# Kernel tuning notes

Hardware: AMD Instinct MI355X
Metric: run time of the kernel (lower is better)

The kernel has to match this reference:

```python
import jax, jax.numpy as jnp
import numpy as np

B, N, DIM = 2, 2048, 2048
N_HEAD, N_KV_HEAD = 32, 8
HEAD_DIM = DIM // N_HEAD  # 64
NEG_INF = -1e9


def setup_inputs() -> dict:
    key = jax.random.key(0)
    ks = jax.random.split(key, 4)
    x = jax.random.normal(ks[0], (B, N, DIM), dtype=jnp.float32)
    Wq = jax.random.normal(ks[1], (DIM, N_HEAD * HEAD_DIM), dtype=jnp.float32) * (DIM ** -0.5)
    Wkv = jax.random.normal(ks[2], (DIM, 2 * N_KV_HEAD * HEAD_DIM), dtype=jnp.float32) * (DIM ** -0.5)
    Wo = jax.random.normal(ks[3], (N_HEAD * HEAD_DIM, DIM), dtype=jnp.float32) * (DIM ** -0.5)
    # RoPE angles: freqs = 1/theta^(2i/d), angle[p, i] = p * freqs[i]
    freqs = 1.0 / (10000.0 ** (jnp.arange(0, HEAD_DIM, 2, dtype=jnp.float32) / HEAD_DIM))
    angles = jnp.arange(N, dtype=jnp.float32)[:, None] * freqs[None, :]  # (N, HEAD_DIM//2)
    rope_cos = jnp.cos(angles)
    rope_sin = jnp.sin(angles)
    # additive causal mask (n, n)
    mask = jnp.where(jnp.tril(jnp.ones((N, N), dtype=bool)), 0.0, NEG_INF).astype(jnp.float32)
    return {"x": x, "Wq": Wq, "Wkv": Wkv, "Wo": Wo, "rope_cos": rope_cos, "rope_sin": rope_sin, "mask": mask, "start_pos": 0}


def apply_rope(x, cos, sin):
    # x: (b, n, h, d); cos/sin: (n, d//2). Complex mult on interleaved pairs.
    xr = x.reshape(*x.shape[:-1], HEAD_DIM // 2, 2)
    xe, xo = xr[..., 0], xr[..., 1]
    c = cos[None, :, None, :]
    s = sin[None, :, None, :]
    yr = xe * c - xo * s
    yi = xe * s + xo * c
    return jnp.stack([yr, yi], axis=-1).reshape(x.shape)


def reference(x, Wq, Wkv, Wo, rope_cos, rope_sin, mask, start_pos):
    b, n, _ = x.shape
    q = (x @ Wq).reshape(b, n, N_HEAD, HEAD_DIM)
    kv = (x @ Wkv).reshape(b, n, 2, N_KV_HEAD, HEAD_DIM)
    k, v = kv[:, :, 0], kv[:, :, 1]
    q = apply_rope(q, rope_cos, rope_sin)
    k = apply_rope(k, rope_cos, rope_sin)
    # repeat kv heads: 'b n h d -> b n (r h) d'
    r = N_HEAD // N_KV_HEAD
    k = jnp.tile(k, (1, 1, r, 1))
    v = jnp.tile(v, (1, 1, r, 1))
    scale = HEAD_DIM ** -0.5
    attn = jnp.einsum('bnhd,bmhd->bhnm', q, k) * scale + mask[None, None]
    attn = jax.nn.softmax(attn, axis=-1)
    out = jnp.einsum('bhnm,bmhd->bnhd', attn, v).reshape(b, n, N_HEAD * HEAD_DIM)
    return out @ Wo
```

## Files before the change

kernel.cpp:

```cpp
#include <hip/hip_runtime.h>


#define BSZ  2
#define NSEQ 2048
#define DIMD 2048
#define NH   32
#define NKV  8
#define HD   64
#define TK   32

typedef __bf16 bf16x8 __attribute__((ext_vector_type(8)));
typedef __bf16 bf16x4 __attribute__((ext_vector_type(4)));
typedef __bf16 bf16x2 __attribute__((ext_vector_type(2)));
typedef float  floatx4 __attribute__((ext_vector_type(4)));

#define MFMA16(a, b, c) __builtin_amdgcn_mfma_f32_16x16x32_bf16(a, b, c, 0, 0, 0)

#define WAITV(n) asm volatile("s_waitcnt vmcnt(" #n ")" ::: "memory")

__device__ __forceinline__ void barrier_nodrain() {
    asm volatile("" ::: "memory");
    __builtin_amdgcn_sched_barrier(0);
    __builtin_amdgcn_s_barrier();
    __builtin_amdgcn_sched_barrier(0);
    asm volatile("" ::: "memory");
}

__device__ __forceinline__ void gload_lds16(const void* g, void* l) {
    __builtin_amdgcn_global_load_lds((const __attribute__((address_space(1))) void*)g,
                                     (__attribute__((address_space(3))) void*)l, 16, 0, 0);
}

__global__ void cvt_x_kernel(const float* __restrict__ in, __bf16* __restrict__ out, int n4) {
    int i = blockIdx.x * blockDim.x + threadIdx.x;
    if (i >= n4) return;
    float4 v = ((const float4*)in)[i];
    bf16x4 o;
    o[0] = (__bf16)v.x; o[1] = (__bf16)v.y; o[2] = (__bf16)v.z; o[3] = (__bf16)v.w;
    ((bf16x4*)out)[i] = o;
}

__global__ void transpose_cvt_kernel(const float* __restrict__ W, __bf16* __restrict__ Wt,
                                     int C, int K) {
    __shared__ float t[32][33];
    int c0 = blockIdx.x * 32, r0 = blockIdx.y * 32;
    int lx = threadIdx.x & 31, ly = threadIdx.x >> 5;
    for (int i = 0; i < 32; i += 8)
        t[ly + i][lx] = W[(size_t)(r0 + ly + i) * C + c0 + lx];
    __syncthreads();
    for (int i = 0; i < 32; i += 8)
        Wt[(size_t)(c0 + ly + i) * K + r0 + lx] = (__bf16)t[lx][ly + i];
}


#define MMAC(mh, nh)                                                           \
    {                                                                          \
        asm volatile("s_waitcnt lgkmcnt(0)" ::: "memory");                     \
        __builtin_amdgcn_sched_barrier(0);                                     \
        __builtin_amdgcn_s_setprio(1);                                         \
        _Pragma("unroll")                                                      \
        for (int il = 0; il < 4; ++il)                                         \
            _Pragma("unroll")                                                  \
            for (int jl = 0; jl < 2; ++jl)                                     \
                _Pragma("unroll")                                              \
                for (int ks = 0; ks < 2; ++ks)                                 \
                    acc[(mh) * 4 + il][(nh) * 2 + jl] =                        \
                        MFMA16(af[il][ks], bfr[jl][ks],                        \
                               acc[(mh) * 4 + il][(nh) * 2 + jl]);             \
        __builtin_amdgcn_s_setprio(0);                                         \
        barrier_nodrain();                                                     \
    }

__device__ __forceinline__ void gemm256_8ph(const __bf16* __restrict__ Ap,
                                            const __bf16* __restrict__ Bp,
                                            __bf16* As, __bf16* Bs,
                                            floatx4 (&acc)[8][4]) {
    int tid = threadIdx.x;
    int wave = tid >> 6, lane = tid & 63;
    int wm = wave >> 2, wn = wave & 3;
    int quad = lane >> 4, l16 = lane & 15;
    int swk = l16 & 7;

    int srcc = ((tid & 7) ^ ((tid >> 3) & 7)) << 3;
    int srow = tid >> 3;
    int wb = wave * 512;

    auto stage = [&](const __bf16* panel, __bf16* region, int kt) {
        gload_lds16(panel + (size_t)srow * DIMD + kt * 64 + srcc, region + wb);
        gload_lds16(panel + (size_t)(64 + srow) * DIMD + kt * 64 + srcc,
                    region + 4096 + wb);
    };

    bf16x8 af[4][2], bfr[2][2];
    auto rdA = [&](const __bf16* R) {
        #pragma unroll
        for (int il = 0; il < 4; ++il) {
            int rl = (2 * il + wm) * 16 + l16;
            #pragma unroll
            for (int ks = 0; ks < 2; ++ks)
                af[il][ks] = *(const bf16x8*)&R[rl * 64 + (((ks * 4 + quad) ^ swk) << 3)];
        }
    };
    auto rdB = [&](const __bf16* R) {
        #pragma unroll
        for (int jl = 0; jl < 2; ++jl) {
            int rl = (4 * jl + wn) * 16 + l16;
            #pragma unroll
            for (int ks = 0; ks < 2; ++ks)
                bfr[jl][ks] = *(const bf16x8*)&R[rl * 64 + (((ks * 4 + quad) ^ swk) << 3)];
        }
    };

    const __bf16* ApH1 = Ap + (size_t)128 * DIMD;
    const __bf16* BpH1 = Bp + (size_t)128 * DIMD;

    stage(Ap,   As + 0,    0);  stage(ApH1, As + 8192, 0);
    stage(Bp,   Bs + 0,    0);  stage(BpH1, Bs + 8192, 0);
    stage(Ap,   As + 16384, 1); stage(BpH1, Bs + 16384 + 8192, 1);

    #pragma unroll 2
    for (int t = 0; t < TK; ++t) {
        int b = t & 1;
        __bf16* Ab  = As + (b << 14);
        __bf16* Bb  = Bs + (b << 14);
        __bf16* Aob = As + ((b ^ 1) << 14);
        __bf16* Bob = Bs + ((b ^ 1) << 14);

        if (t < TK - 1) { WAITV(4); } else { WAITV(0); }
        barrier_nodrain();

        rdA(Ab);
        rdB(Bb);
        if (t + 1 < TK) stage(ApH1, Aob + 8192, t + 1);
        MMAC(0, 0);
        rdB(Bb + 8192);
        if (t + 1 < TK) stage(Bp, Bob, t + 1);
        MMAC(0, 1);
        rdA(Ab + 8192);
        if (t + 2 < TK) stage(Ap, Ab, t + 2);
        MMAC(1, 1);
        rdB(Bb);
        if (t + 2 < TK) stage(BpH1, Bb + 8192, t + 2);
        MMAC(1, 0);
    }
}

#define AROW(i) (((i) >> 2 << 7) + ((2 * ((i) & 3) + wm) << 4) + (quad << 2))
#define BCOL(j) (((j) >> 1 << 7) + ((4 * ((j) & 1) + wn) << 4) + l16)

__global__ __launch_bounds__(512, 2) void gemm_qkv_kernel(
    const __bf16* __restrict__ A, const __bf16* __restrict__ Bt,
    const float* __restrict__ cosb, const float* __restrict__ sinb,
    __bf16* __restrict__ Qo, __bf16* __restrict__ Ko, __bf16* __restrict__ Vo) {
    __shared__ __align__(16) __bf16 As[2 * 2 * 8192];
    __shared__ __align__(16) __bf16 Bs[2 * 2 * 8192];
    int p0 = blockIdx.x * 256;
    int t0 = blockIdx.y * 256;

    floatx4 acc[8][4] = {};
    gemm256_8ph(Bt + (size_t)p0 * DIMD, A + (size_t)t0 * DIMD, As, Bs, acc);

    int tid = threadIdx.x;
    int wave = tid >> 6, lane = tid & 63;
    int wm = wave >> 2, wn = wave & 3;
    int quad = lane >> 4, l16 = lane & 15;
    bool isQ = p0 < 2048;
    bool isV = p0 >= 2560;

    #pragma unroll
    for (int i = 0; i < 8; ++i) {
        int pp = p0 + AROW(i);
        int dq = pp & 63;
        #pragma unroll
        for (int j = 0; j < 4; ++j) {
            int t = t0 + BCOL(j);
            int b = t >> 11, n = t & 2047;
            float x0 = acc[i][j][0], x1 = acc[i][j][1];
            float x2 = acc[i][j][2], x3 = acc[i][j][3];
            if (!isV) {
                int d2 = dq >> 1;
                float2 cv = *(const float2*)(cosb + (size_t)n * 32 + d2);
                float2 sv = *(const float2*)(sinb + (size_t)n * 32 + d2);
                bf16x4 o;
                o[0] = (__bf16)(x0 * cv.x - x1 * sv.x);
                o[1] = (__bf16)(x0 * sv.x + x1 * cv.x);
                o[2] = (__bf16)(x2 * cv.y - x3 * sv.y);
                o[3] = (__bf16)(x2 * sv.y + x3 * cv.y);
                if (isQ) {
                    int h = pp >> 6;
                    *(bf16x4*)&Qo[((size_t)(b * NH + h) * NSEQ + n) * HD + dq] = o;
                } else {
                    int kvh = (pp - 2048) >> 6;
                    *(bf16x4*)&Ko[((size_t)(b * NKV + kvh) * NSEQ + n) * HD + dq] = o;
                }
            } else {
                int kvh = (pp - 2560) >> 6;
                size_t base = (size_t)(b * NKV + kvh) * HD;
                Vo[(base + dq + 0) * NSEQ + n] = (__bf16)x0;
                Vo[(base + dq + 1) * NSEQ + n] = (__bf16)x1;
                Vo[(base + dq + 2) * NSEQ + n] = (__bf16)x2;
                Vo[(base + dq + 3) * NSEQ + n] = (__bf16)x3;
            }
        }
    }
}

__global__ __launch_bounds__(512, 2) void gemm_out_kernel(
    const __bf16* __restrict__ A, const __bf16* __restrict__ Bt,
    float* __restrict__ C) {
    __shared__ __align__(16) __bf16 As[2 * 2 * 8192];
    __shared__ __align__(16) __bf16 Bs[2 * 2 * 8192];
    int n0 = blockIdx.x * 256;
    int m0 = blockIdx.y * 256;

    floatx4 acc[8][4] = {};
    gemm256_8ph(A + (size_t)m0 * DIMD, Bt + (size_t)n0 * DIMD, As, Bs, acc);

    int tid = threadIdx.x;
    int wave = tid >> 6, lane = tid & 63;
    int wm = wave >> 2, wn = wave & 3;
    int quad = lane >> 4, l16 = lane & 15;
    #pragma unroll
    for (int i = 0; i < 8; ++i) {
        int row = m0 + AROW(i);
        #pragma unroll
        for (int j = 0; j < 4; ++j) {
            int col = n0 + BCOL(j);
            float* Cp = C + (size_t)row * 2048 + col;
            Cp[0]    = acc[i][j][0];
            Cp[2048] = acc[i][j][1];
            Cp[4096] = acc[i][j][2];
            Cp[6144] = acc[i][j][3];
        }
    }
}

__global__ __launch_bounds__(256) void attn_kernel(
    const __bf16* __restrict__ Q, const __bf16* __restrict__ K,
    const __bf16* __restrict__ Vt, __bf16* __restrict__ O) {
    __shared__ __align__(16) __bf16 Kl[2][64 * 64];
    __shared__ __align__(16) __bf16 Vl[2][64 * 64];
    __shared__ __align__(16) __bf16 Pl[4][16 * 72];

    int tid = threadIdx.x;
    int wave = tid >> 6, lane = tid & 63;
    int quad = lane >> 4, l16 = lane & 15;
    int bk = blockIdx.x;
    int b = bk >> 3, kvh = bk & 7;
    int h = kvh + wave * 8;

    const __bf16* Qbase = Q + ((size_t)(b * NH + h)) * NSEQ * HD;
    const __bf16* Kbase = K + ((size_t)(b * NKV + kvh)) * NSEQ * HD;
    const __bf16* Vbase = Vt + ((size_t)(b * NKV + kvh)) * HD * NSEQ;
    __bf16* P = &Pl[wave][0];
    const float c2 = 0.125f * 1.44269504f;
    int swk = (l16 & 7) << 3;

    auto stage = [&](int kt, int bi) {
        for (int r = 0; r < 2; ++r) {
            int obase = r * 2048 + wave * 512;
            int o = obase + lane * 8;
            int row = o >> 6;
            int el = (o & 63) ^ ((row & 7) << 3);
            gload_lds16(Kbase + (size_t)kt * 4096 + row * 64 + el, &Kl[bi][obase]);
            gload_lds16(Vbase + (size_t)row * NSEQ + kt * 64 + el, &Vl[bi][obase]);
        }
    };

    int pb = 0;
    stage(0, 0);

    for (int half = 0; half < 2; ++half) {
        int qt = half ? blockIdx.y : 63 - blockIdx.y;
        int q0 = qt * 32;

        bf16x8 qf[2][2];
        for (int s = 0; s < 2; ++s) {
            int qrow = q0 + s * 16 + l16;
            qf[s][0] = *(const bf16x8*)(Qbase + (size_t)qrow * HD + quad * 8);
            qf[s][1] = *(const bf16x8*)(Qbase + (size_t)qrow * HD + 32 + quad * 8);
        }

        floatx4 oa[2][4] = {};
        float l_[2] = {0.0f, 0.0f};
        int ktmax = (q0 + 31) >> 6;

        for (int kt = 0; kt <= ktmax; ++kt) {
            __syncthreads();
            if (kt < ktmax) stage(kt + 1, pb ^ 1);
            else if (half == 0) stage(0, pb ^ 1);

            bf16x8 kf[4][2], vf[4][2];
            for (int j = 0; j < 4; ++j) {
                int rr = (j * 16 + l16) * 64;
                kf[j][0] = *(const bf16x8*)&Kl[pb][rr + ((quad * 8) ^ swk)];
                kf[j][1] = *(const bf16x8*)&Kl[pb][rr + ((quad * 8 + 32) ^ swk)];
                vf[j][0] = *(const bf16x8*)&Vl[pb][rr + ((quad * 8) ^ swk)];
                vf[j][1] = *(const bf16x8*)&Vl[pb][rr + ((quad * 8 + 32) ^ swk)];
            }

            bool diag = (kt == ktmax);
            for (int s = 0; s < 2; ++s) {
                int q_l = q0 + s * 16 + l16;
                for (int j = 0; j < 4; ++j) {
                    floatx4 sv = {0.f, 0.f, 0.f, 0.f};
                    sv = MFMA16(kf[j][0], qf[s][0], sv);
                    sv = MFMA16(kf[j][1], qf[s][1], sv);
                    bf16x4 pk;
                    if (diag) {
                        int kvb = kt * 64 + j * 16 + quad * 4;
                        for (int r = 0; r < 4; ++r) {
                            float p = __builtin_exp2f(sv[r] * c2);
                            if (kvb + r > q_l) p = 0.0f;
                            l_[s] += p;
                            pk[r] = (__bf16)p;
                        }
                    } else {
                        for (int r = 0; r < 4; ++r) {
                            float p = __builtin_exp2f(sv[r] * c2);
                            l_[s] += p;
                            pk[r] = (__bf16)p;
                        }
                    }
                    *(bf16x4*)&P[l16 * 72 + j * 16 + quad * 4] = pk;
                }
                bf16x8 pb0 = *(const bf16x8*)&P[l16 * 72 + quad * 8];
                bf16x8 pb1 = *(const bf16x8*)&P[l16 * 72 + 32 + quad * 8];
                for (int j = 0; j < 4; ++j) {
                    oa[s][j] = MFMA16(vf[j][0], pb0, oa[s][j]);
                    oa[s][j] = MFMA16(vf[j][1], pb1, oa[s][j]);
                }
            }
            pb ^= 1;
        }

        for (int s = 0; s < 2; ++s) {
            float lf = l_[s];
            lf += __shfl_xor(lf, 16, 64);
            lf += __shfl_xor(lf, 32, 64);
            float inv = 1.0f / lf;
            int n = q0 + s * 16 + l16;
            __bf16* Op = O + ((size_t)(b * NSEQ + n)) * (NH * HD) + h * HD + quad * 4;
            for (int j = 0; j < 4; ++j) {
                bf16x4 ov;
                for (int r = 0; r < 4; ++r) ov[r] = (__bf16)(oa[s][j][r] * inv);
                *(bf16x4*)(Op + j * 16) = ov;
            }
        }
    }
}

extern "C" void kernel_launch(void* const* d_in, const int* in_sizes, int n_in,
                              void* d_out, int out_size, void* d_ws, size_t ws_size,
                              hipStream_t stream) {
    const float* x   = (const float*)d_in[0];
    const float* Wq  = (const float*)d_in[1];
    const float* Wkv = (const float*)d_in[2];
    const float* Wo  = (const float*)d_in[3];
    const float* rc  = (const float*)d_in[4];
    const float* rs  = (const float*)d_in[5];
    float* out = (float*)d_out;
    char* ws = (char*)d_ws;

    __bf16* xb    = (__bf16*)(ws + 0);
    __bf16* wqkvt = (__bf16*)(ws + 16777216);
    __bf16* wot   = (__bf16*)(ws + 29360128);
    __bf16* Qb    = (__bf16*)(ws + 37748736);
    __bf16* Kb    = (__bf16*)(ws + 54525952);
    __bf16* Vtb   = (__bf16*)(ws + 58720256);
    __bf16* attnb = (__bf16*)(ws + 62914560);

    cvt_x_kernel<<<8192, 256, 0, stream>>>(x, xb, 2097152);
    transpose_cvt_kernel<<<dim3(64, 64), 256, 0, stream>>>(Wq, wqkvt, 2048, 2048);
    transpose_cvt_kernel<<<dim3(32, 64), 256, 0, stream>>>(Wkv, wqkvt + (size_t)2048 * 2048, 1024, 2048);
    transpose_cvt_kernel<<<dim3(64, 64), 256, 0, stream>>>(Wo, wot, 2048, 2048);

    gemm_qkv_kernel<<<dim3(12, 16), 512, 0, stream>>>(xb, wqkvt, rc, rs, Qb, Kb, Vtb);

    attn_kernel<<<dim3(16, 32), 256, 0, stream>>>(Qb, Kb, Vtb, attnb);

    gemm_out_kernel<<<dim3(8, 16), 512, 0, stream>>>(attnb, wot, out);
}
```

Baseline: 337.5 us.

## Fold softmax scale into Q, compute row sums via MFMA, split attention blocks per q-tile

Folds the softmax scale and log2e into Q during the QKV GEMM epilogue, which removes a multiply per score. Row sums are now accumulated with an MFMA against a ones vector instead of per-lane scalar adds followed by shuffles. The attention kernel now handles one q-tile per block (grid doubled, half-pair balancing dropped) with a launch-bounds occupancy hint. It also swizzles the P buffer in LDS and skips the masked upper half of the diagonal tile. The trade-offs are extra MFMA work for the sums and possible load imbalance without the paired q-tiles.

```diff
diff --git a/kernel.cpp b/kernel.cpp
--- a/kernel.cpp
+++ b/kernel.cpp
@@ -166,6 +166,7 @@
     int quad = lane >> 4, l16 = lane & 15;
     bool isQ = p0 < 2048;
     bool isV = p0 >= 2560;
+    const float sc = isQ ? 0.18033688f : 1.0f;
 
     #pragma unroll
     for (int i = 0; i < 8; ++i) {
@@ -182,10 +183,10 @@
                 float2 cv = *(const float2*)(cosb + (size_t)n * 32 + d2);
                 float2 sv = *(const float2*)(sinb + (size_t)n * 32 + d2);
                 bf16x4 o;
-                o[0] = (__bf16)(x0 * cv.x - x1 * sv.x);
-                o[1] = (__bf16)(x0 * sv.x + x1 * cv.x);
-                o[2] = (__bf16)(x2 * cv.y - x3 * sv.y);
-                o[3] = (__bf16)(x2 * sv.y + x3 * cv.y);
+                o[0] = (__bf16)((x0 * cv.x - x1 * sv.x) * sc);
+                o[1] = (__bf16)((x0 * sv.x + x1 * cv.x) * sc);
+                o[2] = (__bf16)((x2 * cv.y - x3 * sv.y) * sc);
+                o[3] = (__bf16)((x2 * sv.y + x3 * cv.y) * sc);
                 if (isQ) {
                     int h = pp >> 6;
                     *(bf16x4*)&Qo[((size_t)(b * NH + h) * NSEQ + n) * HD + dq] = o;
@@ -235,12 +236,12 @@
     }
 }
 
-__global__ __launch_bounds__(256) void attn_kernel(
+__global__ __launch_bounds__(256, 4) void attn_kernel(
     const __bf16* __restrict__ Q, const __bf16* __restrict__ K,
     const __bf16* __restrict__ Vt, __bf16* __restrict__ O) {
     __shared__ __align__(16) __bf16 Kl[2][64 * 64];
     __shared__ __align__(16) __bf16 Vl[2][64 * 64];
-    __shared__ __align__(16) __bf16 Pl[4][16 * 72];
+    __shared__ __align__(16) __bf16 Pl[4][16 * 64];
 
     int tid = threadIdx.x;
     int wave = tid >> 6, lane = tid & 63;
@@ -248,13 +249,15 @@
     int bk = blockIdx.x;
     int b = bk >> 3, kvh = bk & 7;
     int h = kvh + wave * 8;
+    int qt = 63 - blockIdx.y;
+    int q0 = qt * 32;
 
     const __bf16* Qbase = Q + ((size_t)(b * NH + h)) * NSEQ * HD;
     const __bf16* Kbase = K + ((size_t)(b * NKV + kvh)) * NSEQ * HD;
     const __bf16* Vbase = Vt + ((size_t)(b * NKV + kvh)) * HD * NSEQ;
     __bf16* P = &Pl[wave][0];
-    const float c2 = 0.125f * 1.44269504f;
     int swk = (l16 & 7) << 3;
+    int swp = l16 & 7;
 
     auto stage = [&](int kt, int bi) {
         for (int r = 0; r < 2; ++r) {
@@ -267,85 +270,96 @@
         }
     };
 
+    bf16x8 ones;
+    #pragma unroll
+    for (int t = 0; t < 8; ++t) ones[t] = (__bf16)1.0f;
+
+    bf16x8 qf[2][2];
+    #pragma unroll
+    for (int s = 0; s < 2; ++s) {
+        int qrow = q0 + s * 16 + l16;
+        qf[s][0] = *(const bf16x8*)(Qbase + (size_t)qrow * HD + quad * 8);
+        qf[s][1] = *(const bf16x8*)(Qbase + (size_t)qrow * HD + 32 + quad * 8);
+    }
+
+    floatx4 oa[2][4] = {};
+    floatx4 lacc[2] = {};
+    int ktmax = (q0 + 31) >> 6;
     int pb = 0;
     stage(0, 0);
 
-    for (int half = 0; half < 2; ++half) {
-        int qt = half ? blockIdx.y : 63 - blockIdx.y;
-        int q0 = qt * 32;
-
-        bf16x8 qf[2][2];
+    for (int kt = 0; kt <= ktmax; ++kt) {
+        __syncthreads();
+        if (kt < ktmax) stage(kt + 1, pb ^ 1);
+
+        bool diag = (kt == ktmax);
+        bool half_tile = diag && !(q0 & 32);
+
+        bf16x8 kf[4][2], vf[4][2];
+        #pragma unroll
+        for (int j = 0; j < 4; ++j) {
+            int rr = (j * 16 + l16) * 64;
+            kf[j][0] = *(const bf16x8*)&Kl[pb][rr + ((quad * 8) ^ swk)];
+            kf[j][1] = *(const bf16x8*)&Kl[pb][rr + ((quad * 8 + 32) ^ swk)];
+            vf[j][0] = *(const bf16x8*)&Vl[pb][rr + ((quad * 8) ^ swk)];
+            vf[j][1] = *(const bf16x8*)&Vl[pb][rr + ((quad * 8 + 32) ^ swk)];
+        }
+
+        auto qkj = [&](int j, int s, int q_l) {
+            floatx4 sv = {0.f, 0.f, 0.f, 0.f};
+            sv = MFMA16(kf[j][0], qf[s][0], sv);
+            sv = MFMA16(kf[j][1], qf[s][1], sv);
+            bf16x4 pk;
+            if (diag) {
+                int kvb = kt * 64 + j * 16 + quad * 4;
+                #pragma unroll
+                for (int r = 0; r < 4; ++r) {
+                    float p = __builtin_exp2f(sv[r]);
+                    if (kvb + r > q_l) p = 0.0f;
+                    pk[r] = (__bf16)p;
+                }
+            } else {
+                #pragma unroll
+                for (int r = 0; r < 4; ++r) pk[r] = (__bf16)__builtin_exp2f(sv[r]);
+            }
+            *(bf16x4*)&P[l16 * 64 + ((((j << 1) + (quad >> 1)) ^ swp) << 3) +
+                         ((quad & 1) << 2)] = pk;
+        };
+
+        #pragma unroll
         for (int s = 0; s < 2; ++s) {
-            int qrow = q0 + s * 16 + l16;
-            qf[s][0] = *(const bf16x8*)(Qbase + (size_t)qrow * HD + quad * 8);
-            qf[s][1] = *(const bf16x8*)(Qbase + (size_t)qrow * HD + 32 + quad * 8);
-        }
-
-        floatx4 oa[2][4] = {};
-        float l_[2] = {0.0f, 0.0f};
-        int ktmax = (q0 + 31) >> 6;
-
-        for (int kt = 0; kt <= ktmax; ++kt) {
-            __syncthreads();
-            if (kt < ktmax) stage(kt + 1, pb ^ 1);
-            else if (half == 0) stage(0, pb ^ 1);
-
-            bf16x8 kf[4][2], vf[4][2];
-            for (int j = 0; j < 4; ++j) {
-                int rr = (j * 16 + l16) * 64;
-                kf[j][0] = *(const bf16x8*)&Kl[pb][rr + ((quad * 8) ^ swk)];
-                kf[j][1] = *(const bf16x8*)&Kl[pb][rr + ((quad * 8 + 32) ^ swk)];
-                vf[j][0] = *(const bf16x8*)&Vl[pb][rr + ((quad * 8) ^ swk)];
-                vf[j][1] = *(const bf16x8*)&Vl[pb][rr + ((quad * 8 + 32) ^ swk)];
+            int q_l = q0 + s * 16 + l16;
+            qkj(0, s, q_l);
+            qkj(1, s, q_l);
+            if (!half_tile) { qkj(2, s, q_l); qkj(3, s, q_l); }
+
+            bf16x8 p0 = *(const bf16x8*)&P[l16 * 64 + ((quad ^ swp) << 3)];
+            lacc[s] = MFMA16(ones, p0, lacc[s]);
+            #pragma unroll
+            for (int j = 0; j < 4; ++j)
+                oa[s][j] = MFMA16(vf[j][0], p0, oa[s][j]);
+            if (!half_tile) {
+                bf16x8 p1 = *(const bf16x8*)&P[l16 * 64 + (((4 + quad) ^ swp) << 3)];
+                lacc[s] = MFMA16(ones, p1, lacc[s]);
+                #pragma unroll
+                for (int j = 0; j < 4; ++j)
+                    oa[s][j] = MFMA16(vf[j][1], p1, oa[s][j]);
             }
-
-            bool diag = (kt == ktmax);
-            for (int s = 0; s < 2; ++s) {
-                int q_l = q0 + s * 16 + l16;
-                for (int j = 0; j < 4; ++j) {
-                    floatx4 sv = {0.f, 0.f, 0.f, 0.f};
-                    sv = MFMA16(kf[j][0], qf[s][0], sv);
-                    sv = MFMA16(kf[j][1], qf[s][1], sv);
-                    bf16x4 pk;
-                    if (diag) {
-                        int kvb = kt * 64 + j * 16 + quad * 4;
-                        for (int r = 0; r < 4; ++r) {
-                            float p = __builtin_exp2f(sv[r] * c2);
-                            if (kvb + r > q_l) p = 0.0f;
-                            l_[s] += p;
-                            pk[r] = (__bf16)p;
-                        }
-                    } else {
-                        for (int r = 0; r < 4; ++r) {
-                            float p = __builtin_exp2f(sv[r] * c2);
-                            l_[s] += p;
-                            pk[r] = (__bf16)p;
-                        }
-                    }
-                    *(bf16x4*)&P[l16 * 72 + j * 16 + quad * 4] = pk;
-                }
-                bf16x8 pb0 = *(const bf16x8*)&P[l16 * 72 + quad * 8];
-                bf16x8 pb1 = *(const bf16x8*)&P[l16 * 72 + 32 + quad * 8];
-                for (int j = 0; j < 4; ++j) {
-                    oa[s][j] = MFMA16(vf[j][0], pb0, oa[s][j]);
-                    oa[s][j] = MFMA16(vf[j][1], pb1, oa[s][j]);
-                }
-            }
-            pb ^= 1;
-        }
-
-        for (int s = 0; s < 2; ++s) {
-            float lf = l_[s];
-            lf += __shfl_xor(lf, 16, 64);
-            lf += __shfl_xor(lf, 32, 64);
-            float inv = 1.0f / lf;
-            int n = q0 + s * 16 + l16;
-            __bf16* Op = O + ((size_t)(b * NSEQ + n)) * (NH * HD) + h * HD + quad * 4;
-            for (int j = 0; j < 4; ++j) {
-                bf16x4 ov;
-                for (int r = 0; r < 4; ++r) ov[r] = (__bf16)(oa[s][j][r] * inv);
-                *(bf16x4*)(Op + j * 16) = ov;
-            }
+        }
+        pb ^= 1;
+    }
+
+    #pragma unroll
+    for (int s = 0; s < 2; ++s) {
+        float inv = 1.0f / lacc[s][0];
+        int n = q0 + s * 16 + l16;
+        __bf16* Op = O + ((size_t)(b * NSEQ + n)) * (NH * HD) + h * HD + quad * 4;
+        #pragma unroll
+        for (int j = 0; j < 4; ++j) {
+            bf16x4 ov;
+            #pragma unroll
+            for (int r = 0; r < 4; ++r) ov[r] = (__bf16)(oa[s][j][r] * inv);
+            *(bf16x4*)(Op + j * 16) = ov;
         }
     }
 }
@@ -377,7 +391,7 @@
 
     gemm_qkv_kernel<<<dim3(12, 16), 512, 0, stream>>>(xb, wqkvt, rc, rs, Qb, Kb, Vtb);
 
-    attn_kernel<<<dim3(16, 32), 256, 0, stream>>>(Qb, Kb, Vtb, attnb);
+    attn_kernel<<<dim3(16, 64), 256, 0, stream>>>(Qb, Kb, Vtb, attnb);
 
     gemm_out_kernel<<<dim3(8, 16), 512, 0, stream>>>(attnb, wot, out);
 }
```

Result: slower. 433.1 us (+28.3%).
